# Optimization experiments

Hardware: AMD Instinct MI355X
Metric: run time of the kernel (lower is better)

## Reference

```python
import jax, jax.numpy as jnp
from jax import lax
import numpy as np

NB_HEAD = 8
D_MODEL = 64
KERNEL = 3


def setup_inputs() -> dict:
    key = jax.random.key(0)
    k1, k2, k3, k4, k5 = jax.random.split(key, 5)
    B, N, T, D = 16, 1024, 24, D_MODEL
    value = jax.random.normal(k1, (B, N, T, D), dtype=jnp.float32)
    # Conv2d(d_model, d_model, (1, kernel_size)) weights (OIHW) + bias
    fan_in = D * 1 * KERNEL
    bound = 1.0 / np.sqrt(fan_in)
    W_conv = jax.random.uniform(k2, (D, D, 1, KERNEL), jnp.float32, -bound, bound)
    b_conv = jax.random.uniform(k3, (D,), jnp.float32, -bound, bound)
    # Linear(d_model, d_model): W (out, in), bias (out,)
    lb = 1.0 / np.sqrt(D)
    W_lin = jax.random.uniform(k4, (D, D), jnp.float32, -lb, lb)
    b_lin = jax.random.uniform(k5, (D,), jnp.float32, -lb, lb)
    return {"value": value, "W_conv": W_conv, "b_conv": b_conv,
            "W_lin": W_lin, "b_lin": b_lin}


def reference(value, W_conv, b_conv, W_lin, b_lin):
    B, N, T, D = value.shape
    h = NB_HEAD
    d_k = D // h
    pad = (KERNEL - 1) // 2
    # conv1D_aware_temporal_context1 on value.permute(0,3,1,2): (B, D, N, T)
    x = jnp.transpose(value, (0, 3, 1, 2))
    x = lax.conv_general_dilated(
        x, W_conv, window_strides=(1, 1), padding=[(0, 0), (pad, pad)],
        dimension_numbers=("NCHW", "OIHW", "NCHW"))
    x = x + b_conv[None, :, None, None]
    # view(B, h, d_k, N, T).permute(0,3,1,4,2) -> (B, N, h, T, d_k)
    v = jnp.transpose(x.reshape(B, h, d_k, N, T), (0, 3, 1, 4, 2))
    # relation_matrix_h is the tridiagonal all-ones band -> out[t] = v[t-1]+v[t]+v[t+1]
    vp = jnp.pad(v, ((0, 0), (0, 0), (0, 0), (1, 1), (0, 0)))
    v = vp[..., :-2, :] + vp[..., 1:-1, :] + vp[..., 2:, :]
    # transpose(2,3) then merge heads: (B, N, T, h*d_k)
    v = jnp.transpose(v, (0, 1, 3, 2, 4)).reshape(B, N, T, h * d_k)
    # linear_output1 + relu
    out = jax.nn.relu(jnp.einsum("bntd,od->bnto", v, W_lin) + b_lin)
    return out
```

## Files before the change

kernel.cpp:

```cpp
#include <hip/hip_runtime.h>
#include <hip/hip_bf16.h>


typedef __attribute__((ext_vector_type(8))) short short8;
typedef __attribute__((ext_vector_type(8))) __bf16 bf16x8;
typedef __attribute__((ext_vector_type(4))) float f4;

#define R_ROWS 4
#define VP_STRIDE 72
#define V_ROW_ELEMS (26 * VP_STRIDE)

__device__ __forceinline__ unsigned short f2bfu(float f) {
    return __bfloat16_as_ushort(__float2bfloat16(f));
}

__global__ void prep_kernel(const float* __restrict__ Wconv,
                            const float* __restrict__ bconv,
                            const float* __restrict__ Wlin,
                            const float* __restrict__ blin,
                            __hip_bfloat16* __restrict__ wbig,
                            float* __restrict__ biasC,
                            float* __restrict__ blinF) {
    __shared__ float Wl[4096];
    const int tid = threadIdx.x;
    for (int c = tid; c < 4096; c += 256) Wl[c] = Wlin[c];
    __syncthreads();
    int idx = blockIdx.x * 256 + tid;
    if (idx < 64 * 192) {
        int o = idx / 192;
        int j = idx - o * 192;
        int k = j >> 6;
        int i = j & 63;
        float acc = 0.0f;
        for (int c = 0; c < 64; ++c)
            acc += Wl[o * 64 + c] * Wconv[c * 192 + i * 3 + k];
        wbig[o * 192 + j] = __float2bfloat16(acc);
    } else if (idx < 64 * 192 + 64) {
        int o = idx - 64 * 192;
        float acc = 0.0f;
        for (int c = 0; c < 64; ++c)
            acc += Wl[o * 64 + c] * bconv[c];
        biasC[o] = acc;
    } else if (idx < 64 * 192 + 128) {
        int o = idx - (64 * 192 + 64);
        blinF[o] = blin[o];
    }
}

__global__ __launch_bounds__(256, 6) void fused_kernel(
    const float* __restrict__ value,
    const __hip_bfloat16* __restrict__ wbig,
    const float* __restrict__ biasC,
    const float* __restrict__ blinF,
    float* __restrict__ out) {
    __shared__ __align__(16) short Vlds[R_ROWS * V_ROW_ELEMS];

    const int tid = threadIdx.x;
    const int wave = tid >> 6;
    const int lane = tid & 63;
    const int lane15 = lane & 15;
    const int quad = lane >> 4;
    const long base_row = (long)blockIdx.x * R_ROWS;

    f4 pre[6];
    const int sr = tid >> 6;
    const int tq = (tid >> 4) & 3;
    const int d4 = (tid & 15) << 2;
    {
        const float* vrow = value + base_row * 1536 + sr * 1536 + tq * 64 + d4;
        #pragma unroll
        for (int j = 0; j < 6; ++j)
            pre[j] = *(const f4*)(vrow + j * 256);
    }

    const short* wsrc = (const short*)wbig;
    const int k0 = quad * 8;
    bf16x8 breg[6];
    #pragma unroll
    for (int ks = 0; ks < 6; ++ks)
        breg[ks] = __builtin_bit_cast(bf16x8,
            *(const short8*)(wsrc + (wave * 16 + lane15) * 192 + ks * 32 + k0));

    const int o = wave * 16 + lane15;
    const float bc = biasC[o];
    const float bl = blinF[o];

    if (tid < 64) {
        int r = tid >> 4;
        int which = (tid >> 3) & 1;
        int d8 = (tid & 7) << 3;
        uint4 z; z.x = 0; z.y = 0; z.z = 0; z.w = 0;
        *(uint4*)(Vlds + r * V_ROW_ELEMS + which * (25 * VP_STRIDE) + d8) = z;
    }
    {
        short* lbase = Vlds + sr * V_ROW_ELEMS + (tq + 1) * VP_STRIDE + d4;
        #pragma unroll
        for (int j = 0; j < 6; ++j) {
            ushort4 u;
            u.x = f2bfu(pre[j].x); u.y = f2bfu(pre[j].y);
            u.z = f2bfu(pre[j].z); u.w = f2bfu(pre[j].w);
            *(ushort4*)(lbase + j * (4 * VP_STRIDE)) = u;
        }
    }
    __syncthreads();

    int aoff[6];
    #pragma unroll
    for (int mt = 0; mt < 6; ++mt) {
        int m = mt * 16 + lane15;
        int r = m / 24;
        int s = m - r * 24;
        aoff[mt] = r * V_ROW_ELEMS + s * VP_STRIDE;
    }
    f4 acc[6];
    #pragma unroll
    for (int mt = 0; mt < 6; ++mt) {
        f4 zz = {0.f, 0.f, 0.f, 0.f};
        acc[mt] = zz;
    }
    #pragma unroll
    for (int ks = 0; ks < 6; ++ks) {
        int k = ks * 32 + k0;
        int ka = ((k >> 6) * VP_STRIDE) + (k & 63);
        #pragma unroll
        for (int mt = 0; mt < 6; ++mt) {
            bf16x8 a = __builtin_bit_cast(bf16x8,
                *(const short8*)(Vlds + aoff[mt] + ka));
            acc[mt] = __builtin_amdgcn_mfma_f32_16x16x32_bf16(
                a, breg[ks], acc[mt], 0, 0, 0);
        }
    }

    const float b3 = 3.0f * bc + bl;
    const float b2 = 2.0f * bc + bl;
    const int srcP = (lane + 48) & 63;
    const int srcN = (lane + 16) & 63;
    float* pbase = out + base_row * 1536 + quad * 256 + o;
    #pragma unroll
    for (int mt = 0; mt < 6; ++mt) {
        const int mtp = (mt > 0) ? mt - 1 : 0;
        const int mtn = (mt < 5) ? mt + 1 : 5;
        float sendP = (quad == 3) ? acc[mtp][3] : acc[mt][3];
        float sendN = (quad == 0) ? acc[mtn][0] : acc[mt][0];
        float prev0 = __shfl(sendP, srcP, 64);
        float next3 = __shfl(sendN, srcN, 64);
        const int m3 = mt % 3;
        const bool t0  = (m3 == 0) ? (quad == 0)
                       : ((m3 == 1) ? (quad == 2) : false);
        const bool t23 = (m3 == 2) ? (quad == 3)
                       : ((m3 == 1) ? (quad == 1) : false);
        float s0 = acc[mt][0] + acc[mt][1] + (t0  ? b2 : (prev0 + b3));
        float s1 = acc[mt][0] + acc[mt][1] + acc[mt][2] + b3;
        float s2 = acc[mt][1] + acc[mt][2] + acc[mt][3] + b3;
        float s3 = acc[mt][2] + acc[mt][3] + (t23 ? b2 : (next3 + b3));
        float* p = pbase + mt * 1024;
        p[0]   = fmaxf(s0, 0.0f);
        p[64]  = fmaxf(s1, 0.0f);
        p[128] = fmaxf(s2, 0.0f);
        p[192] = fmaxf(s3, 0.0f);
    }
}

extern "C" void kernel_launch(void* const* d_in, const int* in_sizes, int n_in,
                              void* d_out, int out_size, void* d_ws, size_t ws_size,
                              hipStream_t stream) {
    const float* value = (const float*)d_in[0];
    const float* Wconv = (const float*)d_in[1];
    const float* bconv = (const float*)d_in[2];
    const float* Wlin  = (const float*)d_in[3];
    const float* blin  = (const float*)d_in[4];
    float* out = (float*)d_out;

    __hip_bfloat16* wbig = (__hip_bfloat16*)d_ws;
    float* biasC = (float*)((char*)d_ws + 24576);
    float* blinF = (float*)((char*)d_ws + 24832);

    prep_kernel<<<49, 256, 0, stream>>>(Wconv, bconv, Wlin, blin, wbig, biasC, blinF);
    fused_kernel<<<4096, 256, 0, stream>>>(value, wbig, biasC, blinF, out);
}
```

Measured before the change: 191.7 us.

## Give each wave a private LDS copy of its rows to drop block barrier

Each block now handles two rows instead of four, and every wave loads those two rows into its own private LDS region. This removes the __syncthreads between staging and the MFMA loop. Each wave then computes its 16 output columns over 48 M rows, and the grid doubles. The trade is that all four waves redundantly fetch the same global data, which relies on cache hits and quadruples per-block LDS writes. It also doubles LDS footprint per block and lowers the occupancy hint.

```diff
diff --git a/kernel.cpp b/kernel.cpp
--- a/kernel.cpp
+++ b/kernel.cpp
@@ -6,9 +6,10 @@
 typedef __attribute__((ext_vector_type(8))) __bf16 bf16x8;
 typedef __attribute__((ext_vector_type(4))) float f4;
 
-#define R_ROWS 4
+#define ROWS_PB 2
 #define VP_STRIDE 72
-#define V_ROW_ELEMS (26 * VP_STRIDE)
+#define ROW_SHORTS (26 * VP_STRIDE)
+#define WREG_SHORTS (ROWS_PB * ROW_SHORTS)
 
 __device__ __forceinline__ unsigned short f2bfu(float f) {
     return __bfloat16_as_ushort(__float2bfloat16(f));
@@ -47,30 +48,33 @@
     }
 }
 
-__global__ __launch_bounds__(256, 6) void fused_kernel(
+__global__ __launch_bounds__(256, 4) void fused_kernel(
     const float* __restrict__ value,
     const __hip_bfloat16* __restrict__ wbig,
     const float* __restrict__ biasC,
     const float* __restrict__ blinF,
     float* __restrict__ out) {
-    __shared__ __align__(16) short Vlds[R_ROWS * V_ROW_ELEMS];
+    __shared__ __align__(16) short Vlds[4 * WREG_SHORTS];
 
     const int tid = threadIdx.x;
     const int wave = tid >> 6;
     const int lane = tid & 63;
     const int lane15 = lane & 15;
     const int quad = lane >> 4;
-    const long base_row = (long)blockIdx.x * R_ROWS;
+    const long base_row = (long)blockIdx.x * ROWS_PB;
 
-    f4 pre[6];
-    const int sr = tid >> 6;
-    const int tq = (tid >> 4) & 3;
-    const int d4 = (tid & 15) << 2;
+    short* const wbase = Vlds + wave * WREG_SHORTS;
+
+    f4 pre[12];
+    const int tq = quad;
+    const int d4 = lane15 << 2;
     {
-        const float* vrow = value + base_row * 1536 + sr * 1536 + tq * 64 + d4;
+        const float* vb = value + base_row * 1536 + tq * 64 + d4;
         #pragma unroll
-        for (int j = 0; j < 6; ++j)
-            pre[j] = *(const f4*)(vrow + j * 256);
+        for (int rr = 0; rr < 2; ++rr)
+            #pragma unroll
+            for (int j = 0; j < 6; ++j)
+                pre[rr * 6 + j] = *(const f4*)(vb + rr * 1536 + j * 256);
     }
 
     const short* wsrc = (const short*)wbig;
@@ -85,36 +89,38 @@
     const float bc = biasC[o];
     const float bl = blinF[o];
 
-    if (tid < 64) {
-        int r = tid >> 4;
-        int which = (tid >> 3) & 1;
-        int d8 = (tid & 7) << 3;
+    if (lane < 32) {
+        int rr = (lane >> 4) & 1;
+        int which = (lane >> 3) & 1;
+        int d8 = (lane & 7) << 3;
         uint4 z; z.x = 0; z.y = 0; z.z = 0; z.w = 0;
-        *(uint4*)(Vlds + r * V_ROW_ELEMS + which * (25 * VP_STRIDE) + d8) = z;
+        *(uint4*)(wbase + rr * ROW_SHORTS + which * (25 * VP_STRIDE) + d8) = z;
     }
     {
-        short* lbase = Vlds + sr * V_ROW_ELEMS + (tq + 1) * VP_STRIDE + d4;
+        short* lbase = wbase + (tq + 1) * VP_STRIDE + d4;
         #pragma unroll
-        for (int j = 0; j < 6; ++j) {
-            ushort4 u;
-            u.x = f2bfu(pre[j].x); u.y = f2bfu(pre[j].y);
-            u.z = f2bfu(pre[j].z); u.w = f2bfu(pre[j].w);
-            *(ushort4*)(lbase + j * (4 * VP_STRIDE)) = u;
-        }
+        for (int rr = 0; rr < 2; ++rr)
+            #pragma unroll
+            for (int j = 0; j < 6; ++j) {
+                f4 p = pre[rr * 6 + j];
+                ushort4 u;
+                u.x = f2bfu(p.x); u.y = f2bfu(p.y);
+                u.z = f2bfu(p.z); u.w = f2bfu(p.w);
+                *(ushort4*)(lbase + rr * ROW_SHORTS + j * (4 * VP_STRIDE)) = u;
+            }
     }
-    __syncthreads();
 
-    int aoff[6];
+    int aoff[3];
     #pragma unroll
-    for (int mt = 0; mt < 6; ++mt) {
+    for (int mt = 0; mt < 3; ++mt) {
         int m = mt * 16 + lane15;
-        int r = m / 24;
-        int s = m - r * 24;
-        aoff[mt] = r * V_ROW_ELEMS + s * VP_STRIDE;
+        int rr = m / 24;
+        int s = m - rr * 24;
+        aoff[mt] = rr * ROW_SHORTS + s * VP_STRIDE;
     }
-    f4 acc[6];
+    f4 acc[3];
     #pragma unroll
-    for (int mt = 0; mt < 6; ++mt) {
+    for (int mt = 0; mt < 3; ++mt) {
         f4 zz = {0.f, 0.f, 0.f, 0.f};
         acc[mt] = zz;
     }
@@ -123,9 +129,9 @@
         int k = ks * 32 + k0;
         int ka = ((k >> 6) * VP_STRIDE) + (k & 63);
         #pragma unroll
-        for (int mt = 0; mt < 6; ++mt) {
+        for (int mt = 0; mt < 3; ++mt) {
             bf16x8 a = __builtin_bit_cast(bf16x8,
-                *(const short8*)(Vlds + aoff[mt] + ka));
+                *(const short8*)(wbase + aoff[mt] + ka));
             acc[mt] = __builtin_amdgcn_mfma_f32_16x16x32_bf16(
                 a, breg[ks], acc[mt], 0, 0, 0);
         }
@@ -135,20 +141,19 @@
     const float b2 = 2.0f * bc + bl;
     const int srcP = (lane + 48) & 63;
     const int srcN = (lane + 16) & 63;
-    float* pbase = out + base_row * 1536 + quad * 256 + o;
+    float* pbase = out + (long)blockIdx.x * 3072 + quad * 256 + o;
     #pragma unroll
-    for (int mt = 0; mt < 6; ++mt) {
+    for (int mt = 0; mt < 3; ++mt) {
         const int mtp = (mt > 0) ? mt - 1 : 0;
-        const int mtn = (mt < 5) ? mt + 1 : 5;
+        const int mtn = (mt < 2) ? mt + 1 : 2;
         float sendP = (quad == 3) ? acc[mtp][3] : acc[mt][3];
         float sendN = (quad == 0) ? acc[mtn][0] : acc[mt][0];
         float prev0 = __shfl(sendP, srcP, 64);
         float next3 = __shfl(sendN, srcN, 64);
-        const int m3 = mt % 3;
-        const bool t0  = (m3 == 0) ? (quad == 0)
-                       : ((m3 == 1) ? (quad == 2) : false);
-        const bool t23 = (m3 == 2) ? (quad == 3)
-                       : ((m3 == 1) ? (quad == 1) : false);
+        const bool t0  = (mt == 0) ? (quad == 0)
+                       : ((mt == 1) ? (quad == 2) : false);
+        const bool t23 = (mt == 2) ? (quad == 3)
+                       : ((mt == 1) ? (quad == 1) : false);
         float s0 = acc[mt][0] + acc[mt][1] + (t0  ? b2 : (prev0 + b3));
         float s1 = acc[mt][0] + acc[mt][1] + acc[mt][2] + b3;
         float s2 = acc[mt][1] + acc[mt][2] + acc[mt][3] + b3;
@@ -176,5 +181,5 @@
     float* blinF = (float*)((char*)d_ws + 24832);
 
     prep_kernel<<<49, 256, 0, stream>>>(Wconv, bconv, Wlin, blin, wbig, biasC, blinF);
-    fused_kernel<<<4096, 256, 0, stream>>>(value, wbig, biasC, blinF, out);
+    fused_kernel<<<8192, 256, 0, stream>>>(value, wbig, biasC, blinF, out);
 }
```

Result: slower. 200.3 us (+4.5%).
